# Optimization experiments

Hardware: AMD Instinct MI355X
Metric: run time of the kernel (lower is better)

The kernel has to match this reference:

```python
import jax, jax.numpy as jnp
import numpy as np

N = 8192
IN_FEAT = 256
OUT_FEAT = 128
SLOPE = 0.1
NEG_INF = -9e15


def setup_inputs() -> dict:
    key = jax.random.key(0)
    k_doc, k_Ww, k_Wb, k_aw, k_ab = jax.random.split(key, 5)
    doc = jax.random.normal(k_doc, (N, IN_FEAT), dtype=jnp.float32)
    # nn.Linear(inFeat, outFeat): weight [out, in], bias [out]
    W_w = jax.random.normal(k_Ww, (OUT_FEAT, IN_FEAT), dtype=jnp.float32) / np.sqrt(IN_FEAT)
    W_b = jax.random.normal(k_Wb, (OUT_FEAT,), dtype=jnp.float32) * 0.01
    # nn.Linear(2*outFeat, 1): weight [1, 2*out], bias [1]
    a_w = jax.random.normal(k_aw, (1, 2 * OUT_FEAT), dtype=jnp.float32) / np.sqrt(2 * OUT_FEAT)
    a_b = jax.random.normal(k_ab, (1,), dtype=jnp.float32) * 0.01
    return {"doc": doc, "W_w": W_w, "W_b": W_b, "a_w": a_w, "a_b": a_b, "selfLink": 0}


def reference(doc, W_w, W_b, a_w, a_b, selfLink):
    # h = W(doc)  -> [N, outFeat]
    h = doc @ W_w.T + W_b
    n = h.shape[0]
    # Original builds fch[i, j] = concat(h_i, h_j) -> [N, N, 2D] and applies
    # Linear(2D, 1). Algebraically: score[i,j] = h_i . a_src + h_j . a_dst + b,
    # where a_src/a_dst are the two halves of the weight. Same math, O(N*D) mem.
    a_src = a_w[0, :OUT_FEAT]   # [D]
    a_dst = a_w[0, OUT_FEAT:]   # [D]
    s_src = h @ a_src           # [N]
    s_dst = h @ a_dst           # [N]
    att = jax.nn.leaky_relu(s_src[:, None] + s_dst[None, :] + a_b[0], SLOPE)  # [N, N]
    if selfLink == 0:
        # adj = 1 - eye: mask self-edges
        diag = jnp.eye(n, dtype=bool)
        att = jnp.where(diag, NEG_INF, att)
    att = jax.nn.softmax(att, axis=1)
    h_out = jax.nn.leaky_relu(att @ h, SLOPE)  # [N, D]
    return (h_out, att)
```

## Files before the change

### kernel.cpp

```cpp
#include <hip/hip_runtime.h>
#include <math.h>

#define NROW 8192
#define IN_F 256
#define OUT_F 128
#define SLOPE 0.1f
#define SEGS 256
#define SEGROWS 32

__device__ __forceinline__ float lrelu(float x) { return x > 0.f ? x : SLOPE * x; }

__global__ __launch_bounds__(256) void kA_h_s(const float* __restrict__ doc,
                                              const float* __restrict__ Ww,
                                              const float* __restrict__ Wb,
                                              const float* __restrict__ aw,
                                              float* __restrict__ h,
                                              float* __restrict__ s_src,
                                              float* __restrict__ s_dst,
                                              float* __restrict__ E1,
                                              float* __restrict__ E2) {
    __shared__ float4 sdoc[16][64];
    __shared__ float sred[4][8][2];
    const int t = threadIdx.x;
    const int rowBase = blockIdx.x * 16;
    const float4* doc4 = (const float4*)(doc + (size_t)rowBase * IN_F);
    float4* sflat = &sdoc[0][0];
    for (int i = t; i < 16 * 64; i += 256) sflat[i] = doc4[i];
    __syncthreads();
    const int c = t & 127;
    const int rg = t >> 7;
    float acc[8];
#pragma unroll
    for (int r = 0; r < 8; ++r) acc[r] = 0.f;
    const float4* w4 = (const float4*)(Ww + (size_t)c * IN_F);
    for (int k = 0; k < 64; ++k) {
        const float4 w = w4[k];
#pragma unroll
        for (int r = 0; r < 8; ++r) {
            const float4 d = sdoc[2 * r + rg][k];
            acc[r] += d.x * w.x + d.y * w.y + d.z * w.z + d.w * w.w;
        }
    }
    const float b = Wb[c];
    const float asrc = aw[c];
    const float adst = aw[OUT_F + c];
    const int wave = t >> 6;
    const int lane = t & 63;
#pragma unroll
    for (int r = 0; r < 8; ++r) {
        const float hv = acc[r] + b;
        h[(size_t)(rowBase + 2 * r + rg) * OUT_F + c] = hv;
        float ps = hv * asrc;
        float pd = hv * adst;
        for (int off = 32; off; off >>= 1) {
            ps += __shfl_down(ps, off);
            pd += __shfl_down(pd, off);
        }
        if (lane == 0) { sred[wave][r][0] = ps; sred[wave][r][1] = pd; }
    }
    __syncthreads();
    if (t < 32) {
        const int r = t >> 2;
        const int rem = t & 3;
        const int rg2 = rem >> 1;
        const int which = rem & 1;
        const float val = sred[2 * rg2][r][which] + sred[2 * rg2 + 1][r][which];
        const int row = rowBase + 2 * r + rg2;
        if (which == 0) {
            s_src[row] = val;
        } else {
            s_dst[row] = val;
            E1[row] = expf(val);
            E2[row] = expf(SLOPE * val);
        }
    }
}

__global__ __launch_bounds__(256) void kB_top2(const float* __restrict__ sdst,
                                               float* __restrict__ red) {
    const int t = threadIdx.x;
    float m1 = -1e30f, m2 = -1e30f; int i1 = 0;
    for (int j = t; j < NROW; j += 256) {
        const float v = sdst[j];
        if (v > m1) { m2 = m1; m1 = v; i1 = j; }
        else if (v > m2) { m2 = v; }
    }
    __shared__ float sm1[256], sm2[256];
    __shared__ int si[256];
    sm1[t] = m1; sm2[t] = m2; si[t] = i1;
    __syncthreads();
    for (int s = 128; s > 0; s >>= 1) {
        if (t < s) {
            const float om1 = sm1[t + s], om2 = sm2[t + s];
            const int oi = si[t + s];
            if (om1 > sm1[t]) {
                sm2[t] = fmaxf(sm1[t], om2);
                sm1[t] = om1; si[t] = oi;
            } else {
                sm2[t] = fmaxf(sm2[t], om1);
            }
        }
        __syncthreads();
    }
    if (t == 0) { red[0] = sm1[0]; red[1] = sm2[0]; red[2] = __int_as_float(si[0]); }
}

__global__ __launch_bounds__(256) void kC_rank(const float* __restrict__ sdst,
                                               int* __restrict__ perm) {
    __shared__ float sd[NROW];
    {
        float4* sd4 = (float4*)sd;
        const float4* g4 = (const float4*)sdst;
        for (int q = threadIdx.x; q < NROW / 4; q += 256) sd4[q] = g4[q];
    }
    __syncthreads();
    const int wave = threadIdx.x >> 6, lane = threadIdx.x & 63;
    const int base = blockIdx.x * 32 + wave * 8;
    float rv[8]; int ri[8]; int cnt[8];
#pragma unroll
    for (int r = 0; r < 8; ++r) { ri[r] = base + r; rv[r] = sd[ri[r]]; cnt[r] = 0; }
    for (int j = lane; j < NROW; j += 64) {
        const float v = sd[j];
#pragma unroll
        for (int r = 0; r < 8; ++r)
            cnt[r] += (v < rv[r] || (v == rv[r] && j < ri[r])) ? 1 : 0;
    }
#pragma unroll
    for (int r = 0; r < 8; ++r)
        for (int off = 32; off; off >>= 1) cnt[r] += __shfl_down(cnt[r], off);
    if (lane == 0) {
#pragma unroll
        for (int r = 0; r < 8; ++r) perm[cnt[r]] = ri[r];
    }
}

__global__ __launch_bounds__(256) void kD_gseg(const int* __restrict__ perm,
                                               const float* __restrict__ E1,
                                               const float* __restrict__ E2,
                                               const float* __restrict__ sdst,
                                               const float* __restrict__ h,
                                               float* __restrict__ sortedS,
                                               float* __restrict__ E1s,
                                               float* __restrict__ E2s,
                                               float* __restrict__ seg1,
                                               float* __restrict__ seg2) {
    __shared__ float part[2][4][128][2];
    const int t = threadIdx.x;
    const int c = t & 127;
    const int half = t >> 7;
    const int base = blockIdx.x * 128;
    float a1[4] = {0.f, 0.f, 0.f, 0.f};
    float a2[4] = {0.f, 0.f, 0.f, 0.f};
#pragma unroll
    for (int s = 0; s < 4; ++s) {
        for (int rr2 = 0; rr2 < 16; ++rr2) {
            const int rr = s * 16 + rr2;
            const int lr = rr * 2 + half;
            const int r = base + lr;
            const int i = perm[r];
            const float hv = h[(size_t)i * OUT_F + c];
            const float e1 = E1[i];
            const float e2 = E2[i];
            a1[s] += e1 * hv;
            a2[s] += e2 * hv;
            if (c == 0) { sortedS[r] = sdst[i]; E1s[r] = e1; E2s[r] = e2; }
        }
        part[half][s][c][0] = a1[s];
        part[half][s][c][1] = a2[s];
    }
    __syncthreads();
    const int idx4 = t * 4;
#pragma unroll
    for (int q = 0; q < 4; ++q) {
        const int idx = idx4 + q;
        const int arr = idx & 1;
        const int c2 = (idx >> 1) & 127;
        const int s2 = idx >> 8;
        const float v = part[0][s2][c2][arr] + part[1][s2][c2][arr];
        float* dst = arr ? seg2 : seg1;
        dst[(size_t)(blockIdx.x * 4 + s2) * OUT_F + c2] = v;
    }
}

__global__ __launch_bounds__(256) void kE_scan(const float* __restrict__ seg1,
                                               const float* __restrict__ seg2,
                                               const float* __restrict__ E1s,
                                               const float* __restrict__ E2s,
                                               float* __restrict__ segUo,
                                               float* __restrict__ segVo,
                                               float* __restrict__ Psuf,
                                               float* __restrict__ Qpre) {
    const int p = blockIdx.x;
    const int t = threadIdx.x;
    if (p < 256) {
        const int arr = p >> 7;
        const int col = p & 127;
        const float* src = arr ? seg2 : seg1;
        const float x = src[(size_t)t * OUT_F + col];
        __shared__ float buf[256];
        const int j = arr ? t : (255 - t);
        buf[j] = x;
        __syncthreads();
        for (int off = 1; off < 256; off <<= 1) {
            const float add = (j >= off) ? buf[j - off] : 0.f;
            __syncthreads();
            buf[j] += add;
            __syncthreads();
        }
        const float excl = buf[j] - x;
        float* dst = arr ? segVo : segUo;
        dst[(size_t)t * OUT_F + col] = excl;
    } else if (p == 256) {
        __shared__ float pp[256];
        const int r0 = t * 32;
        float a = 0.f;
        for (int rr = 0; rr < 32; ++rr) a += E1s[r0 + rr];
        pp[t] = a;
        __syncthreads();
        float off = 0.f;
        for (int t2 = t + 1; t2 < 256; ++t2) off += pp[t2];
        float run = off;
        for (int rr = 31; rr >= 0; --rr) { run += E1s[r0 + rr]; Psuf[r0 + rr] = run; }
        if (t == 0) Psuf[NROW] = 0.f;
    } else {
        __shared__ float pp[256];
        const int r0 = t * 32;
        float a = 0.f;
        for (int rr = 0; rr < 32; ++rr) a += E2s[r0 + rr];
        pp[t] = a;
        __syncthreads();
        float off = 0.f;
        for (int t2 = 0; t2 < t; ++t2) off += pp[t2];
        float rv = off;
        for (int rr = 0; rr < 32; ++rr) { Qpre[r0 + rr] = rv; rv += E2s[r0 + rr]; }
        if (t == 255) Qpre[NROW] = rv;
    }
}

__global__ __launch_bounds__(256) void kF_uv(const int* __restrict__ perm,
                                             const float* __restrict__ h,
                                             const float* __restrict__ E1s,
                                             const float* __restrict__ E2s,
                                             const float* __restrict__ segUo,
                                             const float* __restrict__ segVo,
                                             float* __restrict__ U,
                                             float* __restrict__ V) {
    const int t = threadIdx.x;
    const int half = t >> 7;
    const int c = t & 127;
    const int s = blockIdx.x * 2 + half;
    const int r0 = s * SEGROWS;
    float xv[SEGROWS];
#pragma unroll
    for (int rr = 0; rr < SEGROWS; ++rr) {
        const int i = perm[r0 + rr];
        xv[rr] = h[(size_t)i * OUT_F + c];
    }
    float run = segUo[(size_t)s * OUT_F + c];
#pragma unroll
    for (int rr = SEGROWS - 1; rr >= 0; --rr) {
        run += E1s[r0 + rr] * xv[rr];
        U[(size_t)(r0 + rr) * OUT_F + c] = run;
    }
    float rv = segVo[(size_t)s * OUT_F + c];
#pragma unroll
    for (int rr = 0; rr < SEGROWS; ++rr) {
        V[(size_t)(r0 + rr) * OUT_F + c] = rv;
        rv += E2s[r0 + rr] * xv[rr];
    }
    if (s == SEGS - 1) {
        U[(size_t)NROW * OUT_F + c] = 0.f;
        V[(size_t)NROW * OUT_F + c] = rv;
    }
}

__global__ __launch_bounds__(256) void kG_hout(const float* __restrict__ s_src,
                                               const float* __restrict__ sdst,
                                               const float* __restrict__ sortedS,
                                               const float* __restrict__ Psuf,
                                               const float* __restrict__ Qpre,
                                               const float* __restrict__ red,
                                               const float* __restrict__ ab,
                                               const int* __restrict__ selfLink,
                                               const float* __restrict__ U,
                                               const float* __restrict__ V,
                                               const float* __restrict__ h,
                                               float* __restrict__ A,
                                               float* __restrict__ B,
                                               float* __restrict__ rZ,
                                               float* __restrict__ T,
                                               float* __restrict__ hout) {
    const int t = threadIdx.x;
    const int i = blockIdx.x * 2 + (t >> 7);
    const int c = t & 127;
    const bool mask = (selfLink[0] == 0);
    const float tt = s_src[i] + ab[0];
    const float M1 = red[0], M2 = red[1];
    const int i1 = __float_as_int(red[2]);
    const float M = (mask && i1 == i) ? M2 : M1;
    const float m = lrelu(tt + M);
    const float Ai = expf(tt - m);
    const float Bi = expf(SLOPE * tt - m);
    const float eii = mask ? expf(lrelu(tt + sdst[i]) - m) : 0.f;
    const float thr = -tt;
    int lo = 0, hi = NROW;
    while (lo < hi) {
        const int mid = (lo + hi) >> 1;
        if (sortedS[mid] > thr) hi = mid; else lo = mid + 1;
    }
    const int k = lo;
    const float Z = Ai * Psuf[k] + Bi * Qpre[k] - eii;
    const float rZi = 1.f / Z;
    const float val = Ai * U[(size_t)k * OUT_F + c] + Bi * V[(size_t)k * OUT_F + c]
                    - eii * h[(size_t)i * OUT_F + c];
    hout[(size_t)i * OUT_F + c] = lrelu(val * rZi);
    if (c == 0) { A[i] = Ai; B[i] = Bi; rZ[i] = rZi; T[i] = tt; }
}

#define ROWS5 8
#define JCH 2048
__global__ __launch_bounds__(256) void kH_att(const float* __restrict__ sdst,
                                              const float* __restrict__ E1,
                                              const float* __restrict__ E2,
                                              const float* __restrict__ A,
                                              const float* __restrict__ B,
                                              const float* __restrict__ rZ,
                                              const float* __restrict__ T,
                                              const int* __restrict__ selfLink,
                                              float* __restrict__ att) {
    __shared__ float4 sS[JCH / 4], sE1[JCH / 4], sE2[JCH / 4];
    __shared__ float rA[ROWS5], rB[ROWS5], rT[ROWS5];
    const int t = threadIdx.x;
    const int rowBase = blockIdx.x * ROWS5;
    const bool mask = (selfLink[0] == 0);
    if (t < ROWS5) {
        const int i = rowBase + t;
        const float z = rZ[i];
        rA[t] = A[i] * z;
        rB[t] = B[i] * z;
        rT[t] = -T[i];
    }
    for (int ch = 0; ch < NROW; ch += JCH) {
        __syncthreads();
        for (int q = t; q < JCH / 4; q += 256) {
            sS[q]  = ((const float4*)(sdst + ch))[q];
            sE1[q] = ((const float4*)(E1 + ch))[q];
            sE2[q] = ((const float4*)(E2 + ch))[q];
        }
        __syncthreads();
        for (int r = 0; r < ROWS5; ++r) {
            const int i = rowBase + r;
            const float a = rA[r], b = rB[r], thr = rT[r];
            for (int q = t; q < JCH / 4; q += 256) {
                const float4 s4 = sS[q], e1 = sE1[q], e2 = sE2[q];
                float4 o;
                o.x = s4.x > thr ? a * e1.x : b * e2.x;
                o.y = s4.y > thr ? a * e1.y : b * e2.y;
                o.z = s4.z > thr ? a * e1.z : b * e2.z;
                o.w = s4.w > thr ? a * e1.w : b * e2.w;
                const int j0 = ch + q * 4;
                if (mask && i >= j0 && i < j0 + 4) ((float*)&o)[i - j0] = 0.f;
                ((float4*)(att + (size_t)i * NROW + ch))[q] = o;
            }
        }
    }
}

extern "C" void kernel_launch(void* const* d_in, const int* in_sizes, int n_in,
                              void* d_out, int out_size, void* d_ws, size_t ws_size,
                              hipStream_t stream) {
    const float* doc = (const float*)d_in[0];
    const float* Ww  = (const float*)d_in[1];
    const float* Wb  = (const float*)d_in[2];
    const float* aw  = (const float*)d_in[3];
    const float* ab  = (const float*)d_in[4];
    const int* selfLink = (const int*)d_in[5];

    float* out  = (float*)d_out;
    float* hout = out;
    float* att  = out + (size_t)NROW * OUT_F;

    float* h = att;
    float* U = att + 1048576;
    float* V = att + 1048576 + 1048704;

    float* ws = (float*)d_ws;
    float* s_src   = ws;
    float* s_dst   = ws + 8192;
    float* E1      = ws + 16384;
    float* E2      = ws + 24576;
    float* sortedS = ws + 32768;
    float* E1s     = ws + 40960;
    float* E2s     = ws + 49152;
    float* Aarr    = ws + 57344;
    float* Barr    = ws + 65536;
    float* rZ      = ws + 73728;
    float* Tarr    = ws + 81920;
    int*   perm    = (int*)(ws + 90112);
    float* seg1    = ws + 98304;
    float* seg2    = ws + 131072;
    float* segUo   = ws + 163840;
    float* segVo   = ws + 196608;
    float* Psuf    = ws + 229376;
    float* Qpre    = ws + 237632;
    float* red     = ws + 245888;

    kA_h_s <<<512,  256, 0, stream>>>(doc, Ww, Wb, aw, h, s_src, s_dst, E1, E2);
    kB_top2<<<1,    256, 0, stream>>>(s_dst, red);
    kC_rank<<<256,  256, 0, stream>>>(s_dst, perm);
    kD_gseg<<<64,   256, 0, stream>>>(perm, E1, E2, s_dst, h, sortedS, E1s, E2s, seg1, seg2);
    kE_scan<<<258,  256, 0, stream>>>(seg1, seg2, E1s, E2s, segUo, segVo, Psuf, Qpre);
    kF_uv  <<<128,  256, 0, stream>>>(perm, h, E1s, E2s, segUo, segVo, U, V);
    kG_hout<<<4096, 256, 0, stream>>>(s_src, s_dst, sortedS, Psuf, Qpre, red, ab, selfLink,
                                      U, V, h, Aarr, Barr, rZ, Tarr, hout);
    kH_att <<<1024, 256, 0, stream>>>(s_dst, E1, E2, Aarr, Barr, rZ, Tarr, selfLink, att);
}
```

Baseline: 451.3 us.

## Retile projection, merge rank/top2 kernels, widen gather grids, stream att with nontemporal stores

The projection kernel now has each thread compute 4 output columns for 2 rows and reduce the attention dot products with a 32-wide shuffle, which removes the shared-memory reduction pass. The top-2 and rank kernels are merged into one launch. The segment gather and U/V kernels now use one block per segment and stage perm and exp values in shared memory, giving more blocks to spread across CUs. The att writer drops its shared-memory staging, reads s_dst/E1/E2 straight from global memory, covers 16 rows per block and writes with nontemporal stores to cut cache pollution on the 256MB output. Each block now re-reads the column vectors from cache and there are fewer att blocks.

```diff
diff --git a/kernel.cpp b/kernel.cpp
--- a/kernel.cpp
+++ b/kernel.cpp
@@ -7,6 +7,8 @@
 #define SLOPE 0.1f
 #define SEGS 256
 #define SEGROWS 32
+
+typedef float f32x4 __attribute__((ext_vector_type(4)));
 
 __device__ __forceinline__ float lrelu(float x) { return x > 0.f ? x : SLOPE * x; }
 
@@ -20,117 +22,123 @@
                                               float* __restrict__ E1,
                                               float* __restrict__ E2) {
     __shared__ float4 sdoc[16][64];
-    __shared__ float sred[4][8][2];
     const int t = threadIdx.x;
     const int rowBase = blockIdx.x * 16;
     const float4* doc4 = (const float4*)(doc + (size_t)rowBase * IN_F);
     float4* sflat = &sdoc[0][0];
     for (int i = t; i < 16 * 64; i += 256) sflat[i] = doc4[i];
     __syncthreads();
-    const int c = t & 127;
-    const int rg = t >> 7;
-    float acc[8];
-#pragma unroll
-    for (int r = 0; r < 8; ++r) acc[r] = 0.f;
-    const float4* w4 = (const float4*)(Ww + (size_t)c * IN_F);
+    const int cq = t & 31;
+    const int rg = t >> 5;
+    const float4* w0 = (const float4*)(Ww + (size_t)(4 * cq + 0) * IN_F);
+    const float4* w1 = (const float4*)(Ww + (size_t)(4 * cq + 1) * IN_F);
+    const float4* w2 = (const float4*)(Ww + (size_t)(4 * cq + 2) * IN_F);
+    const float4* w3 = (const float4*)(Ww + (size_t)(4 * cq + 3) * IN_F);
+    float a00 = 0.f, a01 = 0.f, a02 = 0.f, a03 = 0.f;
+    float a10 = 0.f, a11 = 0.f, a12 = 0.f, a13 = 0.f;
+#pragma unroll 4
     for (int k = 0; k < 64; ++k) {
-        const float4 w = w4[k];
-#pragma unroll
-        for (int r = 0; r < 8; ++r) {
-            const float4 d = sdoc[2 * r + rg][k];
-            acc[r] += d.x * w.x + d.y * w.y + d.z * w.z + d.w * w.w;
-        }
-    }
-    const float b = Wb[c];
-    const float asrc = aw[c];
-    const float adst = aw[OUT_F + c];
-    const int wave = t >> 6;
-    const int lane = t & 63;
-#pragma unroll
-    for (int r = 0; r < 8; ++r) {
-        const float hv = acc[r] + b;
-        h[(size_t)(rowBase + 2 * r + rg) * OUT_F + c] = hv;
-        float ps = hv * asrc;
-        float pd = hv * adst;
-        for (int off = 32; off; off >>= 1) {
-            ps += __shfl_down(ps, off);
-            pd += __shfl_down(pd, off);
-        }
-        if (lane == 0) { sred[wave][r][0] = ps; sred[wave][r][1] = pd; }
-    }
-    __syncthreads();
-    if (t < 32) {
-        const int r = t >> 2;
-        const int rem = t & 3;
-        const int rg2 = rem >> 1;
-        const int which = rem & 1;
-        const float val = sred[2 * rg2][r][which] + sred[2 * rg2 + 1][r][which];
-        const int row = rowBase + 2 * r + rg2;
-        if (which == 0) {
-            s_src[row] = val;
-        } else {
-            s_dst[row] = val;
-            E1[row] = expf(val);
-            E2[row] = expf(SLOPE * val);
-        }
-    }
-}
-
-__global__ __launch_bounds__(256) void kB_top2(const float* __restrict__ sdst,
-                                               float* __restrict__ red) {
-    const int t = threadIdx.x;
-    float m1 = -1e30f, m2 = -1e30f; int i1 = 0;
-    for (int j = t; j < NROW; j += 256) {
-        const float v = sdst[j];
-        if (v > m1) { m2 = m1; m1 = v; i1 = j; }
-        else if (v > m2) { m2 = v; }
-    }
-    __shared__ float sm1[256], sm2[256];
-    __shared__ int si[256];
-    sm1[t] = m1; sm2[t] = m2; si[t] = i1;
-    __syncthreads();
-    for (int s = 128; s > 0; s >>= 1) {
-        if (t < s) {
-            const float om1 = sm1[t + s], om2 = sm2[t + s];
-            const int oi = si[t + s];
-            if (om1 > sm1[t]) {
-                sm2[t] = fmaxf(sm1[t], om2);
-                sm1[t] = om1; si[t] = oi;
-            } else {
-                sm2[t] = fmaxf(sm2[t], om1);
+        const float4 d0 = sdoc[2 * rg + 0][k];
+        const float4 d1 = sdoc[2 * rg + 1][k];
+        float4 w;
+        w = w0[k];
+        a00 += d0.x * w.x + d0.y * w.y + d0.z * w.z + d0.w * w.w;
+        a10 += d1.x * w.x + d1.y * w.y + d1.z * w.z + d1.w * w.w;
+        w = w1[k];
+        a01 += d0.x * w.x + d0.y * w.y + d0.z * w.z + d0.w * w.w;
+        a11 += d1.x * w.x + d1.y * w.y + d1.z * w.z + d1.w * w.w;
+        w = w2[k];
+        a02 += d0.x * w.x + d0.y * w.y + d0.z * w.z + d0.w * w.w;
+        a12 += d1.x * w.x + d1.y * w.y + d1.z * w.z + d1.w * w.w;
+        w = w3[k];
+        a03 += d0.x * w.x + d0.y * w.y + d0.z * w.z + d0.w * w.w;
+        a13 += d1.x * w.x + d1.y * w.y + d1.z * w.z + d1.w * w.w;
+    }
+    const float4 wb4 = ((const float4*)Wb)[cq];
+    const float4 as4 = ((const float4*)aw)[cq];
+    const float4 ad4 = ((const float4*)(aw + OUT_F))[cq];
+
+#define KA_EPILOG(A0, A1, A2, A3, RR)                                           \
+    do {                                                                        \
+        float4 hv;                                                              \
+        hv.x = (A0) + wb4.x; hv.y = (A1) + wb4.y;                               \
+        hv.z = (A2) + wb4.z; hv.w = (A3) + wb4.w;                               \
+        const int row = rowBase + 2 * rg + (RR);                                \
+        ((float4*)(h + (size_t)row * OUT_F))[cq] = hv;                          \
+        float ps = hv.x * as4.x + hv.y * as4.y + hv.z * as4.z + hv.w * as4.w;   \
+        float pd = hv.x * ad4.x + hv.y * ad4.y + hv.z * ad4.z + hv.w * ad4.w;   \
+        for (int off = 16; off; off >>= 1) {                                    \
+            ps += __shfl_down(ps, off, 32);                                     \
+            pd += __shfl_down(pd, off, 32);                                     \
+        }                                                                       \
+        if (cq == 0) {                                                          \
+            s_src[row] = ps;                                                    \
+            s_dst[row] = pd;                                                    \
+            E1[row] = expf(pd);                                                 \
+            E2[row] = expf(SLOPE * pd);                                         \
+        }                                                                       \
+    } while (0)
+
+    KA_EPILOG(a00, a01, a02, a03, 0);
+    KA_EPILOG(a10, a11, a12, a13, 1);
+#undef KA_EPILOG
+}
+
+__global__ __launch_bounds__(256) void kBC_rank_top2(const float* __restrict__ sdst,
+                                                     float* __restrict__ red,
+                                                     int* __restrict__ perm) {
+    const int t = threadIdx.x;
+    if (blockIdx.x == SEGS) {
+        float m1 = -1e30f, m2 = -1e30f; int i1 = 0;
+        for (int j = t; j < NROW; j += 256) {
+            const float v = sdst[j];
+            if (v > m1) { m2 = m1; m1 = v; i1 = j; }
+            else if (v > m2) { m2 = v; }
+        }
+        __shared__ float sm1[256], sm2[256];
+        __shared__ int si[256];
+        sm1[t] = m1; sm2[t] = m2; si[t] = i1;
+        __syncthreads();
+        for (int s = 128; s > 0; s >>= 1) {
+            if (t < s) {
+                const float om1 = sm1[t + s], om2 = sm2[t + s];
+                const int oi = si[t + s];
+                if (om1 > sm1[t]) {
+                    sm2[t] = fmaxf(sm1[t], om2);
+                    sm1[t] = om1; si[t] = oi;
+                } else {
+                    sm2[t] = fmaxf(sm2[t], om1);
+                }
             }
+            __syncthreads();
+        }
+        if (t == 0) { red[0] = sm1[0]; red[1] = sm2[0]; red[2] = __int_as_float(si[0]); }
+    } else {
+        __shared__ float sd[NROW];
+        {
+            float4* sd4 = (float4*)sd;
+            const float4* g4 = (const float4*)sdst;
+            for (int q = t; q < NROW / 4; q += 256) sd4[q] = g4[q];
         }
         __syncthreads();
-    }
-    if (t == 0) { red[0] = sm1[0]; red[1] = sm2[0]; red[2] = __int_as_float(si[0]); }
-}
-
-__global__ __launch_bounds__(256) void kC_rank(const float* __restrict__ sdst,
-                                               int* __restrict__ perm) {
-    __shared__ float sd[NROW];
-    {
-        float4* sd4 = (float4*)sd;
-        const float4* g4 = (const float4*)sdst;
-        for (int q = threadIdx.x; q < NROW / 4; q += 256) sd4[q] = g4[q];
-    }
-    __syncthreads();
-    const int wave = threadIdx.x >> 6, lane = threadIdx.x & 63;
-    const int base = blockIdx.x * 32 + wave * 8;
-    float rv[8]; int ri[8]; int cnt[8];
-#pragma unroll
-    for (int r = 0; r < 8; ++r) { ri[r] = base + r; rv[r] = sd[ri[r]]; cnt[r] = 0; }
-    for (int j = lane; j < NROW; j += 64) {
-        const float v = sd[j];
+        const int wave = t >> 6, lane = t & 63;
+        const int base = blockIdx.x * 32 + wave * 8;
+        float rv[8]; int ri[8]; int cnt[8];
+#pragma unroll
+        for (int r = 0; r < 8; ++r) { ri[r] = base + r; rv[r] = sd[ri[r]]; cnt[r] = 0; }
+        for (int j = lane; j < NROW; j += 64) {
+            const float v = sd[j];
+#pragma unroll
+            for (int r = 0; r < 8; ++r)
+                cnt[r] += (v < rv[r] || (v == rv[r] && j < ri[r])) ? 1 : 0;
+        }
 #pragma unroll
         for (int r = 0; r < 8; ++r)
-            cnt[r] += (v < rv[r] || (v == rv[r] && j < ri[r])) ? 1 : 0;
-    }
-#pragma unroll
-    for (int r = 0; r < 8; ++r)
-        for (int off = 32; off; off >>= 1) cnt[r] += __shfl_down(cnt[r], off);
-    if (lane == 0) {
-#pragma unroll
-        for (int r = 0; r < 8; ++r) perm[cnt[r]] = ri[r];
+            for (int off = 32; off; off >>= 1) cnt[r] += __shfl_down(cnt[r], off);
+        if (lane == 0) {
+#pragma unroll
+            for (int r = 0; r < 8; ++r) perm[cnt[r]] = ri[r];
+        }
     }
 }
 
@@ -144,41 +152,40 @@
                                                float* __restrict__ E2s,
                                                float* __restrict__ seg1,
                                                float* __restrict__ seg2) {
-    __shared__ float part[2][4][128][2];
-    const int t = threadIdx.x;
+    __shared__ int sp[SEGROWS];
+    __shared__ float se1[SEGROWS], se2[SEGROWS];
+    __shared__ float part[2][OUT_F][2];
+    const int t = threadIdx.x;
+    const int s = blockIdx.x;
+    const int r0 = s * SEGROWS;
+    if (t < SEGROWS) {
+        const int i = perm[r0 + t];
+        sp[t] = i;
+        const float e1 = E1[i], e2 = E2[i];
+        se1[t] = e1; se2[t] = e2;
+        sortedS[r0 + t] = sdst[i];
+        E1s[r0 + t] = e1;
+        E2s[r0 + t] = e2;
+    }
+    __syncthreads();
     const int c = t & 127;
     const int half = t >> 7;
-    const int base = blockIdx.x * 128;
-    float a1[4] = {0.f, 0.f, 0.f, 0.f};
-    float a2[4] = {0.f, 0.f, 0.f, 0.f};
-#pragma unroll
-    for (int s = 0; s < 4; ++s) {
-        for (int rr2 = 0; rr2 < 16; ++rr2) {
-            const int rr = s * 16 + rr2;
-            const int lr = rr * 2 + half;
-            const int r = base + lr;
-            const int i = perm[r];
-            const float hv = h[(size_t)i * OUT_F + c];
-            const float e1 = E1[i];
-            const float e2 = E2[i];
-            a1[s] += e1 * hv;
-            a2[s] += e2 * hv;
-            if (c == 0) { sortedS[r] = sdst[i]; E1s[r] = e1; E2s[r] = e2; }
-        }
-        part[half][s][c][0] = a1[s];
-        part[half][s][c][1] = a2[s];
-    }
+    float a1 = 0.f, a2 = 0.f;
+#pragma unroll
+    for (int rr2 = 0; rr2 < 16; ++rr2) {
+        const int rr = half * 16 + rr2;
+        const float hv = h[(size_t)sp[rr] * OUT_F + c];
+        a1 += se1[rr] * hv;
+        a2 += se2[rr] * hv;
+    }
+    part[half][c][0] = a1;
+    part[half][c][1] = a2;
     __syncthreads();
-    const int idx4 = t * 4;
-#pragma unroll
-    for (int q = 0; q < 4; ++q) {
-        const int idx = idx4 + q;
-        const int arr = idx & 1;
-        const int c2 = (idx >> 1) & 127;
-        const int s2 = idx >> 8;
-        const float v = part[0][s2][c2][arr] + part[1][s2][c2][arr];
-        float* dst = arr ? seg2 : seg1;
-        dst[(size_t)(blockIdx.x * 4 + s2) * OUT_F + c2] = v;
+    if (t < 128) {
+        seg1[(size_t)s * OUT_F + t] = part[0][t][0] + part[1][t][0];
+    } else {
+        const int c2 = t - 128;
+        seg2[(size_t)s * OUT_F + c2] = part[0][c2][1] + part[1][c2][1];
     }
 }
 
@@ -245,32 +252,42 @@
                                              const float* __restrict__ segVo,
                                              float* __restrict__ U,
                                              float* __restrict__ V) {
-    const int t = threadIdx.x;
-    const int half = t >> 7;
+    __shared__ int sp[SEGROWS];
+    __shared__ float se1[SEGROWS], se2[SEGROWS];
+    __shared__ float sUo[OUT_F], sVo[OUT_F];
+    const int t = threadIdx.x;
+    const int s = blockIdx.x;
+    const int r0 = s * SEGROWS;
+    if (t < 128) sUo[t] = segUo[(size_t)s * OUT_F + t];
+    else         sVo[t - 128] = segVo[(size_t)s * OUT_F + (t - 128)];
+    if (t < SEGROWS) {
+        sp[t] = perm[r0 + t];
+        se1[t] = E1s[r0 + t];
+        se2[t] = E2s[r0 + t];
+    }
+    __syncthreads();
     const int c = t & 127;
-    const int s = blockIdx.x * 2 + half;
-    const int r0 = s * SEGROWS;
+    const int doV = t >> 7;
     float xv[SEGROWS];
 #pragma unroll
-    for (int rr = 0; rr < SEGROWS; ++rr) {
-        const int i = perm[r0 + rr];
-        xv[rr] = h[(size_t)i * OUT_F + c];
-    }
-    float run = segUo[(size_t)s * OUT_F + c];
-#pragma unroll
-    for (int rr = SEGROWS - 1; rr >= 0; --rr) {
-        run += E1s[r0 + rr] * xv[rr];
-        U[(size_t)(r0 + rr) * OUT_F + c] = run;
-    }
-    float rv = segVo[(size_t)s * OUT_F + c];
-#pragma unroll
-    for (int rr = 0; rr < SEGROWS; ++rr) {
-        V[(size_t)(r0 + rr) * OUT_F + c] = rv;
-        rv += E2s[r0 + rr] * xv[rr];
-    }
-    if (s == SEGS - 1) {
-        U[(size_t)NROW * OUT_F + c] = 0.f;
-        V[(size_t)NROW * OUT_F + c] = rv;
+    for (int rr = 0; rr < SEGROWS; ++rr)
+        xv[rr] = h[(size_t)sp[rr] * OUT_F + c];
+    if (!doV) {
+        float run = sUo[c];
+#pragma unroll
+        for (int rr = SEGROWS - 1; rr >= 0; --rr) {
+            run += se1[rr] * xv[rr];
+            U[(size_t)(r0 + rr) * OUT_F + c] = run;
+        }
+        if (s == SEGS - 1) U[(size_t)NROW * OUT_F + c] = 0.f;
+    } else {
+        float rv = sVo[c];
+#pragma unroll
+        for (int rr = 0; rr < SEGROWS; ++rr) {
+            V[(size_t)(r0 + rr) * OUT_F + c] = rv;
+            rv += se2[rr] * xv[rr];
+        }
+        if (s == SEGS - 1) V[(size_t)NROW * OUT_F + c] = rv;
     }
 }
 
@@ -317,8 +334,7 @@
     if (c == 0) { A[i] = Ai; B[i] = Bi; rZ[i] = rZi; T[i] = tt; }
 }
 
-#define ROWS5 8
-#define JCH 2048
+#define RH 16
 __global__ __launch_bounds__(256) void kH_att(const float* __restrict__ sdst,
                                               const float* __restrict__ E1,
                                               const float* __restrict__ E2,
@@ -328,40 +344,44 @@
                                               const float* __restrict__ T,
                                               const int* __restrict__ selfLink,
                                               float* __restrict__ att) {
-    __shared__ float4 sS[JCH / 4], sE1[JCH / 4], sE2[JCH / 4];
-    __shared__ float rA[ROWS5], rB[ROWS5], rT[ROWS5];
-    const int t = threadIdx.x;
-    const int rowBase = blockIdx.x * ROWS5;
-    const bool mask = (selfLink[0] == 0);
-    if (t < ROWS5) {
+    __shared__ float rA[RH], rB[RH], rT[RH];
+    const int t = threadIdx.x;
+    const int rowBase = blockIdx.x * RH;
+    if (t < RH) {
         const int i = rowBase + t;
         const float z = rZ[i];
         rA[t] = A[i] * z;
         rB[t] = B[i] * z;
         rT[t] = -T[i];
     }
-    for (int ch = 0; ch < NROW; ch += JCH) {
-        __syncthreads();
-        for (int q = t; q < JCH / 4; q += 256) {
-            sS[q]  = ((const float4*)(sdst + ch))[q];
-            sE1[q] = ((const float4*)(E1 + ch))[q];
-            sE2[q] = ((const float4*)(E2 + ch))[q];
-        }
-        __syncthreads();
-        for (int r = 0; r < ROWS5; ++r) {
+    __syncthreads();
+    const bool mask = (selfLink[0] == 0);
+    const f32x4* s4p = (const f32x4*)sdst;
+    const f32x4* e1p = (const f32x4*)E1;
+    const f32x4* e2p = (const f32x4*)E2;
+    for (int it = 0; it < NROW / (4 * 256); ++it) {
+        const int q = it * 256 + t;
+        const f32x4 s4 = s4p[q];
+        const f32x4 e1 = e1p[q];
+        const f32x4 e2 = e2p[q];
+        const int j0 = q * 4;
+#pragma unroll
+        for (int r = 0; r < RH; ++r) {
+            const float a = rA[r], b = rB[r], thr = rT[r];
+            f32x4 o;
+            o.x = s4.x > thr ? a * e1.x : b * e2.x;
+            o.y = s4.y > thr ? a * e1.y : b * e2.y;
+            o.z = s4.z > thr ? a * e1.z : b * e2.z;
+            o.w = s4.w > thr ? a * e1.w : b * e2.w;
             const int i = rowBase + r;
-            const float a = rA[r], b = rB[r], thr = rT[r];
-            for (int q = t; q < JCH / 4; q += 256) {
-                const float4 s4 = sS[q], e1 = sE1[q], e2 = sE2[q];
-                float4 o;
-                o.x = s4.x > thr ? a * e1.x : b * e2.x;
-                o.y = s4.y > thr ? a * e1.y : b * e2.y;
-                o.z = s4.z > thr ? a * e1.z : b * e2.z;
-                o.w = s4.w > thr ? a * e1.w : b * e2.w;
-                const int j0 = ch + q * 4;
-                if (mask && i >= j0 && i < j0 + 4) ((float*)&o)[i - j0] = 0.f;
-                ((float4*)(att + (size_t)i * NROW + ch))[q] = o;
+            const int d = i - j0;
+            if (mask && ((unsigned)d < 4u)) {
+                if (d == 0) o.x = 0.f;
+                else if (d == 1) o.y = 0.f;
+                else if (d == 2) o.z = 0.f;
+                else o.w = 0.f;
             }
+            __builtin_nontemporal_store(o, (f32x4*)(att + (size_t)i * NROW) + q);
         }
     }
 }
@@ -405,13 +425,12 @@
     float* Qpre    = ws + 237632;
     float* red     = ws + 245888;
 
-    kA_h_s <<<512,  256, 0, stream>>>(doc, Ww, Wb, aw, h, s_src, s_dst, E1, E2);
-    kB_top2<<<1,    256, 0, stream>>>(s_dst, red);
-    kC_rank<<<256,  256, 0, stream>>>(s_dst, perm);
-    kD_gseg<<<64,   256, 0, stream>>>(perm, E1, E2, s_dst, h, sortedS, E1s, E2s, seg1, seg2);
-    kE_scan<<<258,  256, 0, stream>>>(seg1, seg2, E1s, E2s, segUo, segVo, Psuf, Qpre);
-    kF_uv  <<<128,  256, 0, stream>>>(perm, h, E1s, E2s, segUo, segVo, U, V);
-    kG_hout<<<4096, 256, 0, stream>>>(s_src, s_dst, sortedS, Psuf, Qpre, red, ab, selfLink,
-                                      U, V, h, Aarr, Barr, rZ, Tarr, hout);
-    kH_att <<<1024, 256, 0, stream>>>(s_dst, E1, E2, Aarr, Barr, rZ, Tarr, selfLink, att);
-}
+    kA_h_s       <<<512,  256, 0, stream>>>(doc, Ww, Wb, aw, h, s_src, s_dst, E1, E2);
+    kBC_rank_top2<<<257,  256, 0, stream>>>(s_dst, red, perm);
+    kD_gseg      <<<256,  256, 0, stream>>>(perm, E1, E2, s_dst, h, sortedS, E1s, E2s, seg1, seg2);
+    kE_scan      <<<258,  256, 0, stream>>>(seg1, seg2, E1s, E2s, segUo, segVo, Psuf, Qpre);
+    kF_uv        <<<256,  256, 0, stream>>>(perm, h, E1s, E2s, segUo, segVo, U, V);
+    kG_hout      <<<4096, 256, 0, stream>>>(s_src, s_dst, sortedS, Psuf, Qpre, red, ab, selfLink,
+                                            U, V, h, Aarr, Barr, rZ, Tarr, hout);
+    kH_att       <<<512,  256, 0, stream>>>(s_dst, E1, E2, Aarr, Barr, rZ, Tarr, selfLink, att);
+}
```

Measured after the change: 426.0 us. 1.06x faster.
